# Performance work log

Hardware: AMD Instinct MI355X
Metric: run time of the kernel (lower is better)

Reference implementation:

```python
import jax, jax.numpy as jnp
import numpy as np

N_EMBD = 1024

def setup_inputs() -> dict:
    key = jax.random.key(0)
    ks = jax.random.split(key, 7)
    x = jax.random.normal(ks[0], (4, 2048, N_EMBD), dtype=jnp.float32)
    s = 1.0 / np.sqrt(N_EMBD)
    Wk = jax.random.normal(ks[1], (N_EMBD, N_EMBD), dtype=jnp.float32) * s
    bk = jnp.zeros((N_EMBD,), dtype=jnp.float32)
    Wq = jax.random.normal(ks[2], (N_EMBD, N_EMBD), dtype=jnp.float32) * s
    bq = jnp.zeros((N_EMBD,), dtype=jnp.float32)
    Wv = jax.random.normal(ks[3], (N_EMBD, N_EMBD), dtype=jnp.float32) * s
    bv = jnp.zeros((N_EMBD,), dtype=jnp.float32)
    return {"x": x, "Wk": Wk, "bk": bk, "Wq": Wq, "bq": bq, "Wv": Wv, "bv": bv}

def reference(x, Wk, bk, Wq, bq, Wv, bv):
    B, T, C = x.shape
    k = x @ Wk.T + bk  # [B,T,C]
    q = x @ Wq.T + bq
    v = x @ Wv.T + bv
    # scaled scores with causal mask (note: original scales by C**-0.5)
    scores = jnp.einsum('btc,bsc->bts', q, k) * (C ** -0.5)  # [B,T,T]
    causal = jnp.tril(jnp.ones((T, T), dtype=bool))
    scores = jnp.where(causal, scores, -jnp.inf)
    weights = jax.nn.softmax(scores, axis=-1)
    # dropout disabled (inference mode)
    y = jnp.einsum('bts,bsc->btc', weights, v)
    return y
```

## Files before the change

kernel.cpp:

```cpp
#include <hip/hip_runtime.h>
#include <hip/hip_bf16.h>

typedef __attribute__((ext_vector_type(8))) short short8;
typedef __attribute__((ext_vector_type(4))) float f32x4;

__device__ __forceinline__ ushort f2b(float f) {
    __hip_bfloat16 h = __float2bfloat16(f);
    return *reinterpret_cast<ushort*>(&h);
}
__device__ __forceinline__ float b2f(ushort u) {
    return __uint_as_float(((unsigned)u) << 16);
}
__device__ __forceinline__ void gload16(const ushort* g, ushort* l) {
    __builtin_amdgcn_global_load_lds(
        (const __attribute__((address_space(1))) void*)g,
        (__attribute__((address_space(3))) void*)l, 16, 0, 0);
}

template <int MODE>
__global__ __launch_bounds__(256, 3) void gemm_ring(
    const ushort* __restrict__ xb, const ushort* __restrict__ Wcat,
    const float* __restrict__ bk, const float* __restrict__ bq, const float* __restrict__ bv,
    ushort* __restrict__ Kb, ushort* __restrict__ Qb, ushort* __restrict__ Vt,
    ushort* __restrict__ Sb, float* __restrict__ out) {
    constexpr int T = 2048, C = 1024;
    __shared__ ushort smem[24576];

    const int tid = threadIdx.x;
    const int l = tid & 63, w = tid >> 6;
    const int wm = (w >> 1) * 64, wn = (w & 1) * 64;
    const int lr = l & 15, lk = l >> 4;

    int m0, n0, nt, iblk = 0, jblk = 0, z = 0;
    const ushort *Au, *Bu;
    int ldA, ldB;
    if constexpr (MODE == 0) {
        const int wg = blockIdx.x;
        const int swz = (wg & 7) * 192 + (wg >> 3);
        m0 = (swz / 24) * 128; n0 = (swz % 24) * 128;
        Au = xb + (size_t)m0 * C;   ldA = C;
        Bu = Wcat + (size_t)n0 * C; ldB = C;
        nt = 32;
    } else if constexpr (MODE == 1) {
        const int wg0 = blockIdx.x;
        const int wg = (wg0 & 7) * 68 + (wg0 >> 3);
        z = wg / 136; const int t136 = wg % 136;
        int i = (int)((sqrtf(8.f * t136 + 1.f) - 1.f) * 0.5f);
        while ((i + 1) * (i + 2) / 2 <= t136) ++i;
        while (i * (i + 1) / 2 > t136) --i;
        const int j = t136 - i * (i + 1) / 2;
        iblk = i; jblk = j;
        m0 = i * 128; n0 = j * 128;
        Au = Qb + (size_t)z * T * C + (size_t)m0 * C; ldA = C;
        Bu = Kb + (size_t)z * T * C + (size_t)m0 * 0 + (size_t)(j * 128) * C; ldB = C;
        nt = 32;
    } else {
        const int wg0 = blockIdx.x;
        const int wg = (wg0 & 7) * 64 + (wg0 >> 3);
        const int half = wg >> 8, s2 = wg & 255;
        z = s2 >> 6; const int r6 = s2 & 63;
        const int nb = r6 & 7, ii = r6 >> 3;
        const int i = half ? (15 - ii) : ii;
        iblk = i;
        m0 = i * 128; n0 = nb * 128;
        Au = Sb + (size_t)z * T * T + (size_t)m0 * T; ldA = T;
        Bu = Vt + (size_t)z * C * T + (size_t)n0 * T; ldB = T;
        nt = 4 * (i + 1);
    }

    const int srow = w * 16 + (l >> 2);
    const int scb = ((l & 3) << 4) ^ ((l >= 32) ? 32 : 0);
    const ushort* gA = Au + (size_t)srow * ldA + (scb >> 1);
    const ushort* gB = Bu + (size_t)srow * ldB + (scb >> 1);
    const size_t a64 = (size_t)64 * ldA, b64 = (size_t)64 * ldB;
    const int LBu = lr * 32 + ((lk << 3) ^ ((lr >= 8) ? 16 : 0));

    f32x4 acc[4][4] = {};

#define STAGE(tt, sl)                                                    \
    {                                                                    \
        const int _ko = (tt) * 32;                                       \
        ushort* _d = smem + (sl) * 8192 + w * 512;                       \
        gload16(gA + _ko,        _d);                                    \
        gload16(gA + a64 + _ko,  _d + 2048);                             \
        gload16(gB + _ko,        _d + 4096);                             \
        gload16(gB + b64 + _ko,  _d + 6144);                             \
    }

    STAGE(0, 0);
    STAGE(1, 1);
    asm volatile("s_waitcnt vmcnt(4)" ::: "memory");
    __builtin_amdgcn_s_barrier();
    asm volatile("" ::: "memory");

    int sc = 0, ss = 2;
    for (int t = 0; t < nt; ++t) {
        const ushort* As = smem + sc * 8192 + (wm >> 4) * 512 + LBu;
        const ushort* Bs = smem + sc * 8192 + 4096 + (wn >> 4) * 512 + LBu;
        short8 af[4], bf[4];
#pragma unroll
        for (int q = 0; q < 4; ++q) {
            af[q] = *reinterpret_cast<const short8*>(As + q * 512);
            bf[q] = *reinterpret_cast<const short8*>(Bs + q * 512);
        }
        if (t + 2 < nt) STAGE(t + 2, ss);
        __builtin_amdgcn_s_setprio(1);
#pragma unroll
        for (int mf = 0; mf < 4; ++mf)
#pragma unroll
            for (int nf = 0; nf < 4; ++nf)
                acc[mf][nf] = __builtin_amdgcn_mfma_f32_16x16x32_bf16(af[mf], bf[nf], acc[mf][nf], 0, 0, 0);
        __builtin_amdgcn_s_setprio(0);
        if (t + 1 < nt) {
            if (t + 2 < nt) asm volatile("s_waitcnt vmcnt(4)" ::: "memory");
            else            asm volatile("s_waitcnt vmcnt(0)" ::: "memory");
            __builtin_amdgcn_s_barrier();
            asm volatile("" ::: "memory");
        }
        sc = (sc == 2) ? 0 : sc + 1;
        ss = (ss == 2) ? 0 : ss + 1;
    }
#undef STAGE

    if constexpr (MODE == 0) {
        const int zsel = n0 >> 10;
        const int c0 = (n0 & 1023) + wn;
        if (zsel < 2) {
            ushort* O = (zsel == 0) ? Kb : Qb;
            const float* bias = (zsel == 0) ? bk : bq;
#pragma unroll
            for (int mf = 0; mf < 4; ++mf)
#pragma unroll
                for (int nf = 0; nf < 4; ++nf) {
                    const int gc = c0 + nf * 16 + lr;
                    const float badd = bias[gc];
#pragma unroll
                    for (int rr = 0; rr < 4; ++rr) {
                        const int gr = m0 + wm + mf * 16 + lk * 4 + rr;
                        O[(size_t)gr * C + gc] = f2b(acc[mf][nf][rr] + badd);
                    }
                }
        } else {
            const int zb = (m0 + wm) >> 11;
            const int s0 = (m0 + wm) & 2047;
            ushort* Vz = Vt + (size_t)zb * C * T;
#pragma unroll
            for (int mf = 0; mf < 4; ++mf)
#pragma unroll
                for (int nf = 0; nf < 4; ++nf) {
                    const int gc = c0 + nf * 16 + lr;
                    const float badd = bv[gc];
                    const int s = s0 + mf * 16 + lk * 4;
                    ushort tmp[4];
#pragma unroll
                    for (int rr = 0; rr < 4; ++rr) tmp[rr] = f2b(acc[mf][nf][rr] + badd);
                    *reinterpret_cast<uint2*>(Vz + (size_t)gc * T + s) =
                        *reinterpret_cast<uint2*>(tmp);
                }
        }
    } else if constexpr (MODE == 1) {
        ushort* Sp = Sb + (size_t)z * T * T;
        const bool diag = (iblk == jblk);
#pragma unroll
        for (int mf = 0; mf < 4; ++mf)
#pragma unroll
            for (int nf = 0; nf < 4; ++nf) {
                const int gc = n0 + wn + nf * 16 + lr;
#pragma unroll
                for (int rr = 0; rr < 4; ++rr) {
                    const int gr = m0 + wm + mf * 16 + lk * 4 + rr;
                    if (!diag || gc <= gr)
                        Sp[(size_t)gr * T + gc] = f2b(acc[mf][nf][rr] * 0.03125f);
                }
            }
    } else {
        float* Op = out + (size_t)z * T * C;
#pragma unroll
        for (int mf = 0; mf < 4; ++mf)
#pragma unroll
            for (int nf = 0; nf < 4; ++nf) {
                const int gc = n0 + wn + nf * 16 + lr;
#pragma unroll
                for (int rr = 0; rr < 4; ++rr) {
                    const int gr = m0 + wm + mf * 16 + lk * 4 + rr;
                    Op[(size_t)gr * C + gc] = acc[mf][nf][rr];
                }
            }
    }
}

__global__ __launch_bounds__(256) void cvt_all(
    const float* __restrict__ x, const float* __restrict__ Wk,
    const float* __restrict__ Wq, const float* __restrict__ Wv,
    ushort* __restrict__ xb, ushort* __restrict__ Wcat) {
    constexpr int C = 1024;
    constexpr int NX = 8388608 / 8, NW = C * C / 8;
    int i = blockIdx.x * 256 + threadIdx.x;
    const float* src; ushort* dst;
    if (i < NX)               { src = x;  dst = xb; }
    else if (i < NX + NW)     { src = Wk; dst = Wcat;                 i -= NX; }
    else if (i < NX + 2 * NW) { src = Wq; dst = Wcat + (size_t)C * C; i -= NX + NW; }
    else                      { src = Wv; dst = Wcat + 2 * (size_t)C * C; i -= NX + 2 * NW; }
    const float4* p = reinterpret_cast<const float4*>(src) + (size_t)i * 2;
    float4 a = p[0], b = p[1];
    ushort o[8] = {f2b(a.x), f2b(a.y), f2b(a.z), f2b(a.w),
                   f2b(b.x), f2b(b.y), f2b(b.z), f2b(b.w)};
    reinterpret_cast<uint4*>(dst)[i] = *reinterpret_cast<uint4*>(o);
}

__global__ __launch_bounds__(256) void softmax_rows(ushort* __restrict__ S, int T) {
    const int g = blockIdx.x;
    const int r = g & (T - 1);
    ushort* p = S + (size_t)g * T;
    const int tid = threadIdx.x;
    const int lane = tid & 63, wave = tid >> 6;
    const int c0 = tid * 8;
    const int n_write = ((r >> 7) + 1) << 7;

    float f[8];
    if (c0 <= r) {
        uint4 raw = *reinterpret_cast<const uint4*>(p + c0);
        ushort* rs = reinterpret_cast<ushort*>(&raw);
#pragma unroll
        for (int j = 0; j < 8; ++j) f[j] = (c0 + j <= r) ? b2f(rs[j]) : -INFINITY;
    } else {
#pragma unroll
        for (int j = 0; j < 8; ++j) f[j] = -INFINITY;
    }

    float mx = f[0];
#pragma unroll
    for (int j = 1; j < 8; ++j) mx = fmaxf(mx, f[j]);
#pragma unroll
    for (int o = 32; o > 0; o >>= 1) mx = fmaxf(mx, __shfl_xor(mx, o));

    __shared__ float redm[4], reds[4];
    if (lane == 0) redm[wave] = mx;
    __syncthreads();
    mx = fmaxf(fmaxf(redm[0], redm[1]), fmaxf(redm[2], redm[3]));

    float e[8], s = 0.f;
#pragma unroll
    for (int j = 0; j < 8; ++j) { e[j] = __expf(f[j] - mx); s += e[j]; }
#pragma unroll
    for (int o = 32; o > 0; o >>= 1) s += __shfl_xor(s, o);
    if (lane == 0) reds[wave] = s;
    __syncthreads();
    s = reds[0] + reds[1] + reds[2] + reds[3];

    const float inv = 1.f / s;
    if (c0 < n_write) {
        ushort outv[8];
#pragma unroll
        for (int j = 0; j < 8; ++j) outv[j] = f2b(e[j] * inv);
        *reinterpret_cast<uint4*>(p + c0) = *reinterpret_cast<uint4*>(outv);
    }
}

extern "C" void kernel_launch(void* const* d_in, const int* in_sizes, int n_in,
                              void* d_out, int out_size, void* d_ws, size_t ws_size,
                              hipStream_t stream) {
    const float* x  = (const float*)d_in[0];
    const float* Wk = (const float*)d_in[1];
    const float* bk = (const float*)d_in[2];
    const float* Wq = (const float*)d_in[3];
    const float* bq = (const float*)d_in[4];
    const float* Wv = (const float*)d_in[5];
    const float* bv = (const float*)d_in[6];
    float* out = (float*)d_out;

    constexpr int B = 4, T = 2048, C = 1024;
    constexpr size_t BTC = (size_t)B * T * C;

    ushort* Kb = (ushort*)d_ws;
    ushort* Qb = Kb + BTC;
    ushort* Vt = Qb + BTC;
    ushort* Sb = Vt + BTC;
    ushort* xb   = Sb;
    ushort* Wcat = Sb + BTC;

    dim3 blk(256);

    cvt_all<<<dim3(5632), blk, 0, stream>>>(x, Wk, Wq, Wv, xb, Wcat);

    gemm_ring<0><<<dim3(1536), blk, 0, stream>>>(xb, Wcat, bk, bq, bv,
                                                 Kb, Qb, Vt, Sb, out);

    gemm_ring<1><<<dim3(544), blk, 0, stream>>>(xb, Wcat, bk, bq, bv,
                                                Kb, Qb, Vt, Sb, out);

    softmax_rows<<<dim3(B * T), blk, 0, stream>>>(Sb, T);

    gemm_ring<2><<<dim3(512), blk, 0, stream>>>(xb, Wcat, bk, bq, bv,
                                                Kb, Qb, Vt, Sb, out);
}
```

Baseline: 153.7 us.

## Replace QKV projection GEMM with dedicated 256x128-tile 512-thread kernel

The fused QKV projection moves out of the templated ring GEMM into its own kernel. It uses 256x128 output tiles, 8 waves per block, and a two-buffer double-K-substep pipeline in 96 KB of LDS. The larger tile raises arithmetic intensity and cuts the number of global loads of x and W per output, at the cost of occupancy of one block per CU and more accumulator registers per wave. The remaining ring kernel drops its unused mode-0 path and takes a smaller argument list.

```diff
diff --git a/kernel.cpp b/kernel.cpp
--- a/kernel.cpp
+++ b/kernel.cpp
@@ -17,12 +17,131 @@
         (__attribute__((address_space(3))) void*)l, 16, 0, 0);
 }
 
+__global__ __launch_bounds__(512, 1) void qkv_gemm256(
+    const ushort* __restrict__ xb, const ushort* __restrict__ Wcat,
+    const float* __restrict__ bk, const float* __restrict__ bq, const float* __restrict__ bv,
+    ushort* __restrict__ Kb, ushort* __restrict__ Qb, ushort* __restrict__ Vt) {
+    constexpr int T = 2048, C = 1024, K = 1024, NT = 16;
+    __shared__ ushort smem[49152];
+
+    const int tid = threadIdx.x;
+    const int l = tid & 63, w = tid >> 6;
+    const int wm = (w >> 2) * 128, wn = (w & 3) * 32;
+    const int lr = l & 15, lk = l >> 4;
+
+    const int b = blockIdx.x;
+    const int wg = (b & 7) * 96 + (b >> 3);
+    const int m0 = (wg / 24) * 256, n0 = (wg % 24) * 128;
+
+    const int srow = w * 16 + (l >> 2);
+    const int scb = ((l & 3) << 4) ^ ((l & 32) ? 32 : 0);
+    const ushort* gA = xb + (size_t)(m0 + srow) * K + (scb >> 1);
+    const ushort* gB = Wcat + (size_t)(n0 + srow) * K + (scb >> 1);
+
+    const int LB = lr * 32 + ((lk << 3) ^ ((lr >= 8) ? 16 : 0));
+
+    f32x4 acc[8][2] = {};
+
+#define STAGEQ(u1, ks)                                                    \
+    {                                                                     \
+        ushort* _base = smem + ((u1) & 1) * 24576 + (ks) * 12288;         \
+        const int _ko = (u1) * 64 + (ks) * 32;                            \
+        ushort* _da = _base + w * 512;                                    \
+        gload16(gA + _ko, _da);                                           \
+        gload16(gA + (size_t)128 * K + _ko, _da + 4096);                  \
+        gload16(gB + _ko, _base + 8192 + w * 512);                        \
+    }
+
+    STAGEQ(0, 0);
+    STAGEQ(0, 1);
+
+    for (int u = 0; u < NT; ++u) {
+        const ushort* buf = smem + (u & 1) * 24576;
+        asm volatile("s_waitcnt vmcnt(3)" ::: "memory");
+        __builtin_amdgcn_s_barrier();
+        asm volatile("" ::: "memory");
+        {
+            const ushort* Ab = buf + (wm >> 4) * 512 + LB;
+            const ushort* Bb = buf + 8192 + (wn >> 4) * 512 + LB;
+            short8 a[8], bf2[2];
+#pragma unroll
+            for (int f = 0; f < 8; ++f) a[f] = *reinterpret_cast<const short8*>(Ab + f * 512);
+            bf2[0] = *reinterpret_cast<const short8*>(Bb);
+            bf2[1] = *reinterpret_cast<const short8*>(Bb + 512);
+            if (u + 1 < NT) STAGEQ(u + 1, 0);
+            __builtin_amdgcn_s_setprio(1);
+#pragma unroll
+            for (int f = 0; f < 8; ++f)
+#pragma unroll
+                for (int g = 0; g < 2; ++g)
+                    acc[f][g] = __builtin_amdgcn_mfma_f32_16x16x32_bf16(a[f], bf2[g], acc[f][g], 0, 0, 0);
+            __builtin_amdgcn_s_setprio(0);
+        }
+        if (u + 1 < NT) asm volatile("s_waitcnt vmcnt(3)" ::: "memory");
+        else            asm volatile("s_waitcnt vmcnt(0)" ::: "memory");
+        __builtin_amdgcn_s_barrier();
+        asm volatile("" ::: "memory");
+        {
+            const ushort* Ab = buf + 12288 + (wm >> 4) * 512 + LB;
+            const ushort* Bb = buf + 12288 + 8192 + (wn >> 4) * 512 + LB;
+            short8 a[8], bf2[2];
+#pragma unroll
+            for (int f = 0; f < 8; ++f) a[f] = *reinterpret_cast<const short8*>(Ab + f * 512);
+            bf2[0] = *reinterpret_cast<const short8*>(Bb);
+            bf2[1] = *reinterpret_cast<const short8*>(Bb + 512);
+            if (u + 1 < NT) STAGEQ(u + 1, 1);
+            __builtin_amdgcn_s_setprio(1);
+#pragma unroll
+            for (int f = 0; f < 8; ++f)
+#pragma unroll
+                for (int g = 0; g < 2; ++g)
+                    acc[f][g] = __builtin_amdgcn_mfma_f32_16x16x32_bf16(a[f], bf2[g], acc[f][g], 0, 0, 0);
+            __builtin_amdgcn_s_setprio(0);
+        }
+    }
+#undef STAGEQ
+
+    const int zsel = n0 >> 10;
+    const int c0 = (n0 & 1023) + wn;
+    if (zsel < 2) {
+        ushort* O = (zsel == 0) ? Kb : Qb;
+        const float* bias = (zsel == 0) ? bk : bq;
+#pragma unroll
+        for (int f = 0; f < 8; ++f)
+#pragma unroll
+            for (int g = 0; g < 2; ++g) {
+                const int gc = c0 + g * 16 + lr;
+                const float badd = bias[gc];
+#pragma unroll
+                for (int rr = 0; rr < 4; ++rr) {
+                    const int gr = m0 + wm + f * 16 + lk * 4 + rr;
+                    O[(size_t)gr * C + gc] = f2b(acc[f][g][rr] + badd);
+                }
+            }
+    } else {
+        const int zb = (m0 + wm) >> 11;
+        const int s0 = (m0 + wm) & 2047;
+        ushort* Vz = Vt + (size_t)zb * C * T;
+#pragma unroll
+        for (int f = 0; f < 8; ++f)
+#pragma unroll
+            for (int g = 0; g < 2; ++g) {
+                const int gc = c0 + g * 16 + lr;
+                const float badd = bv[gc];
+                const int s = s0 + f * 16 + lk * 4;
+                ushort tmp[4];
+#pragma unroll
+                for (int rr = 0; rr < 4; ++rr) tmp[rr] = f2b(acc[f][g][rr] + badd);
+                *reinterpret_cast<uint2*>(Vz + (size_t)gc * T + s) =
+                    *reinterpret_cast<uint2*>(tmp);
+            }
+    }
+}
+
 template <int MODE>
 __global__ __launch_bounds__(256, 3) void gemm_ring(
-    const ushort* __restrict__ xb, const ushort* __restrict__ Wcat,
-    const float* __restrict__ bk, const float* __restrict__ bq, const float* __restrict__ bv,
-    ushort* __restrict__ Kb, ushort* __restrict__ Qb, ushort* __restrict__ Vt,
-    ushort* __restrict__ Sb, float* __restrict__ out) {
+    const ushort* __restrict__ Kb, const ushort* __restrict__ Qb,
+    const ushort* __restrict__ Vt, ushort* __restrict__ Sb, float* __restrict__ out) {
     constexpr int T = 2048, C = 1024;
     __shared__ ushort smem[24576];
 
@@ -34,14 +153,7 @@
     int m0, n0, nt, iblk = 0, jblk = 0, z = 0;
     const ushort *Au, *Bu;
     int ldA, ldB;
-    if constexpr (MODE == 0) {
-        const int wg = blockIdx.x;
-        const int swz = (wg & 7) * 192 + (wg >> 3);
-        m0 = (swz / 24) * 128; n0 = (swz % 24) * 128;
-        Au = xb + (size_t)m0 * C;   ldA = C;
-        Bu = Wcat + (size_t)n0 * C; ldB = C;
-        nt = 32;
-    } else if constexpr (MODE == 1) {
+    if constexpr (MODE == 1) {
         const int wg0 = blockIdx.x;
         const int wg = (wg0 & 7) * 68 + (wg0 >> 3);
         z = wg / 136; const int t136 = wg % 136;
@@ -52,7 +164,7 @@
         iblk = i; jblk = j;
         m0 = i * 128; n0 = j * 128;
         Au = Qb + (size_t)z * T * C + (size_t)m0 * C; ldA = C;
-        Bu = Kb + (size_t)z * T * C + (size_t)m0 * 0 + (size_t)(j * 128) * C; ldB = C;
+        Bu = Kb + (size_t)z * T * C + (size_t)n0 * C; ldB = C;
         nt = 32;
     } else {
         const int wg0 = blockIdx.x;
@@ -122,43 +234,7 @@
     }
 #undef STAGE
 
-    if constexpr (MODE == 0) {
-        const int zsel = n0 >> 10;
-        const int c0 = (n0 & 1023) + wn;
-        if (zsel < 2) {
-            ushort* O = (zsel == 0) ? Kb : Qb;
-            const float* bias = (zsel == 0) ? bk : bq;
-#pragma unroll
-            for (int mf = 0; mf < 4; ++mf)
-#pragma unroll
-                for (int nf = 0; nf < 4; ++nf) {
-                    const int gc = c0 + nf * 16 + lr;
-                    const float badd = bias[gc];
-#pragma unroll
-                    for (int rr = 0; rr < 4; ++rr) {
-                        const int gr = m0 + wm + mf * 16 + lk * 4 + rr;
-                        O[(size_t)gr * C + gc] = f2b(acc[mf][nf][rr] + badd);
-                    }
-                }
-        } else {
-            const int zb = (m0 + wm) >> 11;
-            const int s0 = (m0 + wm) & 2047;
-            ushort* Vz = Vt + (size_t)zb * C * T;
-#pragma unroll
-            for (int mf = 0; mf < 4; ++mf)
-#pragma unroll
-                for (int nf = 0; nf < 4; ++nf) {
-                    const int gc = c0 + nf * 16 + lr;
-                    const float badd = bv[gc];
-                    const int s = s0 + mf * 16 + lk * 4;
-                    ushort tmp[4];
-#pragma unroll
-                    for (int rr = 0; rr < 4; ++rr) tmp[rr] = f2b(acc[mf][nf][rr] + badd);
-                    *reinterpret_cast<uint2*>(Vz + (size_t)gc * T + s) =
-                        *reinterpret_cast<uint2*>(tmp);
-                }
-        }
-    } else if constexpr (MODE == 1) {
+    if constexpr (MODE == 1) {
         ushort* Sp = Sb + (size_t)z * T * T;
         const bool diag = (iblk == jblk);
 #pragma unroll
@@ -283,14 +359,11 @@
 
     cvt_all<<<dim3(5632), blk, 0, stream>>>(x, Wk, Wq, Wv, xb, Wcat);
 
-    gemm_ring<0><<<dim3(1536), blk, 0, stream>>>(xb, Wcat, bk, bq, bv,
-                                                 Kb, Qb, Vt, Sb, out);
-
-    gemm_ring<1><<<dim3(544), blk, 0, stream>>>(xb, Wcat, bk, bq, bv,
-                                                Kb, Qb, Vt, Sb, out);
+    qkv_gemm256<<<dim3(768), dim3(512), 0, stream>>>(xb, Wcat, bk, bq, bv, Kb, Qb, Vt);
+
+    gemm_ring<1><<<dim3(544), blk, 0, stream>>>(Kb, Qb, Vt, Sb, out);
 
     softmax_rows<<<dim3(B * T), blk, 0, stream>>>(Sb, T);
 
-    gemm_ring<2><<<dim3(512), blk, 0, stream>>>(xb, Wcat, bk, bq, bv,
-                                                Kb, Qb, Vt, Sb, out);
-}
+    gemm_ring<2><<<dim3(512), blk, 0, stream>>>(Kb, Qb, Vt, Sb, out);
+}
```

Result: faster. 145.6 us (-5.3%).
